# Performance work log

Hardware: AMD Instinct MI355X
Metric: run time of the kernel (lower is better)

Reference implementation:

```python
import jax, jax.numpy as jnp
import numpy as np

HIDDEN = 4096
N_HEADS = 32
HEAD_DIM = HIDDEN // N_HEADS  # 128
ROPE_BASE = 10000.0
NEG_INF = -1e9  # stands in for torch.finfo(dtype).min in the additive mask


def rotate_half(x):
    x1 = x[..., : x.shape[-1] // 2]
    x2 = x[..., x.shape[-1] // 2 :]
    return jnp.concatenate((-x2, x1), axis=-1)


def rope_tables(seq_len, dtype=jnp.float32):
    # RotaryEmbedding: inv_freq = 1/base^(arange(0,dim,2)/dim); emb = cat(freqs, freqs)
    inv_freq = 1.0 / (ROPE_BASE ** (jnp.arange(0, HEAD_DIM, 2, dtype=jnp.float32) / HEAD_DIM))
    t = jnp.arange(seq_len, dtype=jnp.float32)
    freqs = jnp.einsum('s,d->sd', t, inv_freq)          # [S, HEAD_DIM/2]
    emb = jnp.concatenate((freqs, freqs), axis=-1)      # [S, HEAD_DIM]
    return jnp.cos(emb).astype(dtype), jnp.sin(emb).astype(dtype)


def setup_inputs() -> dict:
    key = jax.random.key(0)
    k0, k1, k2 = jax.random.split(key, 3)
    B, S = 1, 2048
    hidden_states = jax.random.normal(k0, (B, S, HIDDEN), dtype=jnp.float32)
    W_pack = jax.random.normal(k1, (3 * HIDDEN, HIDDEN), dtype=jnp.float32) * 0.02
    W_o = jax.random.normal(k2, (HIDDEN, HIDDEN), dtype=jnp.float32) * 0.02
    position_ids = jnp.broadcast_to(jnp.arange(S, dtype=jnp.int32)[None, :], (B, S))
    # additive causal mask [B, 1, S, S]
    causal = jnp.tril(jnp.ones((S, S), dtype=bool))
    attention_mask = jnp.where(causal, 0.0, NEG_INF).astype(jnp.float32)[None, None, :, :]
    attention_mask = jnp.broadcast_to(attention_mask, (B, 1, S, S))
    return {
        'hidden_states': hidden_states,
        'attention_mask': attention_mask,
        'position_ids': position_ids,
        'W_pack': W_pack,
        'W_o': W_o,
    }


def reference(hidden_states, attention_mask, position_ids, W_pack, W_o):
    B, S, H = hidden_states.shape
    norm_factor = 1.0 / np.sqrt(HEAD_DIM)

    # fused QKV projection: Linear(H, 3H, bias=False)
    proj = jnp.einsum('bsh,ph->bsp', hidden_states, W_pack)        # [B, S, 3H]
    q, k, v = jnp.split(proj, 3, axis=-1)

    def to_heads(x):
        return x.reshape(B, S, N_HEADS, HEAD_DIM).transpose(0, 2, 1, 3)  # [B, nH, S, D]

    q, k, v = to_heads(q), to_heads(k), to_heads(v)

    # RoPE (gather per position_ids, matching apply_rotary_pos_emb with unsqueeze_dim=1)
    cos_t, sin_t = rope_tables(S, hidden_states.dtype)
    cos = cos_t[position_ids][:, None, :, :]  # [B, 1, S, D]
    sin = sin_t[position_ids][:, None, :, :]
    q = q * cos + rotate_half(q) * sin
    k = k * cos + rotate_half(k) * sin

    # manual QK^T / softmax / AV (prefill: KV-cache update is a plain copy of cur)
    scores = jnp.einsum('bhqd,bhkd->bhqk', q, k) * norm_factor + attention_mask
    probs = jax.nn.softmax(scores, axis=-1)
    attn = jnp.einsum('bhqk,bhkd->bhqd', probs, v)                 # [B, nH, S, D]

    attn = attn.transpose(0, 2, 1, 3).reshape(B, S, H)
    return jnp.einsum('bsh,oh->bso', attn, W_o)
```

## Files before the change

### kernel.cpp

```cpp
#include <hip/hip_runtime.h>
#include <math.h>

typedef __bf16 bf16x8 __attribute__((ext_vector_type(8)));
typedef __bf16 bf16x4 __attribute__((ext_vector_type(4)));
typedef float f32x4 __attribute__((ext_vector_type(4)));

#define S_LEN 2048
#define NHEADS 32
#define DHEAD 128
#define HID 4096

__device__ __forceinline__ void gld16(const void* g, void* l) {
  __builtin_amdgcn_global_load_lds(
      (const __attribute__((address_space(1))) unsigned int*)g,
      (__attribute__((address_space(3))) unsigned int*)l, 16, 0, 0);
}

__global__ __launch_bounds__(256) void cvt_k(const float4* __restrict__ in,
                                             __bf16* __restrict__ out, int n4) {
  int i = blockIdx.x * 256 + threadIdx.x;
  if (i >= n4) return;
  float4 f = in[i];
  bf16x4 o;
  o[0] = (__bf16)f.x; o[1] = (__bf16)f.y; o[2] = (__bf16)f.z; o[3] = (__bf16)f.w;
  *(bf16x4*)(out + (size_t)i * 4) = o;
}

template <int ND, int KD, int EPI>
__global__ __launch_bounds__(256) void gemm_bt(const __bf16* __restrict__ A,
                                               const __bf16* __restrict__ B,
                                               float* __restrict__ C,
                                               __bf16* __restrict__ Qh,
                                               __bf16* __restrict__ Kh,
                                               __bf16* __restrict__ Vh) {
  const int bn = blockIdx.x, bm = blockIdx.y;
  const int t = threadIdx.x;
  const int w = t >> 6, l = t & 63, quad = l >> 4, l15 = l & 15;
  const int wr = w >> 1, wc = w & 1;

  __shared__ __align__(16) __bf16 As[128 * 32];
  __shared__ __align__(16) __bf16 Bs[128 * 32];

  const f32x4 zero4 = {0.f, 0.f, 0.f, 0.f};
  f32x4 acc[4][4];
#pragma unroll
  for (int i = 0; i < 4; ++i)
#pragma unroll
    for (int j = 0; j < 4; ++j) acc[i][j] = zero4;

  const __bf16* Ab = A + (size_t)bm * 128 * KD;
  const __bf16* Bb = B + (size_t)bn * 128 * KD;

  for (int k0 = 0; k0 < KD; k0 += 32) {
    __syncthreads();
#pragma unroll
    for (int j = 0; j < 2; ++j) {
      const int c = j * 256 + t;
      const int row = c >> 2, kcs = c & 3;
      const int kc = (kcs - (row >> 1)) & 3;
      const int cb = j * 256 + w * 64;
      gld16(Ab + (size_t)row * KD + k0 + kc * 8, As + (size_t)cb * 8);
      gld16(Bb + (size_t)row * KD + k0 + kc * 8, Bs + (size_t)cb * 8);
    }
    __syncthreads();
    bf16x8 af[4], bf_[4];
    const int cq = (quad + (l15 >> 1)) & 3;
#pragma unroll
    for (int mi = 0; mi < 4; ++mi)
      af[mi] = *(const bf16x8*)(As + (wr * 64 + mi * 16 + l15) * 32 + cq * 8);
#pragma unroll
    for (int ni = 0; ni < 4; ++ni)
      bf_[ni] = *(const bf16x8*)(Bs + (wc * 64 + ni * 16 + l15) * 32 + cq * 8);
#pragma unroll
    for (int mi = 0; mi < 4; ++mi)
#pragma unroll
      for (int ni = 0; ni < 4; ++ni)
        acc[mi][ni] = __builtin_amdgcn_mfma_f32_16x16x32_bf16(af[mi], bf_[ni], acc[mi][ni], 0, 0, 0);
  }

#pragma unroll
  for (int mi = 0; mi < 4; ++mi)
#pragma unroll
    for (int ni = 0; ni < 4; ++ni)
#pragma unroll
      for (int r = 0; r < 4; ++r) {
        const int row = bm * 128 + wr * 64 + mi * 16 + quad * 4 + r;
        const int col = bn * 128 + wc * 64 + ni * 16 + l15;
        const float v = acc[mi][ni][r];
        if constexpr (EPI == 0) {
          C[(size_t)row * ND + col] = v;
        } else {
          const int part = col >> 12;
          const int cl = col & 4095;
          const int hh = cl >> 7, d = cl & 127;
          __bf16* dst = (part == 0) ? Qh : (part == 1) ? Kh : Vh;
          dst[(size_t)(hh * S_LEN + row) * DHEAD + d] = (__bf16)v;
        }
      }
}

__global__ __launch_bounds__(256) void rope_k(__bf16* __restrict__ Q, __bf16* __restrict__ K) {
  const int idx = blockIdx.x * 256 + threadIdx.x;
  const int i = idx & 63;
  const int s = (idx >> 6) & (S_LEN - 1);
  const int h = idx >> 17;
  const float inv_freq = __expf(-9.210340371976184f * (float)i * (1.0f / 64.0f));
  float sn, cs;
  sincosf((float)s * inv_freq, &sn, &cs);
  const float nf = 0.08838834764831845f;
  const size_t base = (size_t)(h * S_LEN + s) * DHEAD;
  const float q0 = (float)Q[base + i], q1 = (float)Q[base + i + 64];
  Q[base + i]      = (__bf16)((q0 * cs - q1 * sn) * nf);
  Q[base + i + 64] = (__bf16)((q1 * cs + q0 * sn) * nf);
  const float k0 = (float)K[base + i], k1 = (float)K[base + i + 64];
  K[base + i]      = (__bf16)(k0 * cs - k1 * sn);
  K[base + i + 64] = (__bf16)(k1 * cs + k0 * sn);
}

__global__ __launch_bounds__(256) void vtrans_k(const __bf16* __restrict__ Vh,
                                                __bf16* __restrict__ Vt) {
  __shared__ __align__(16) __bf16 tile[64][72];
  const int s0 = blockIdx.x * 64, d0 = blockIdx.y * 64, h = blockIdx.z;
  const int t = threadIdx.x;
#pragma unroll
  for (int j = 0; j < 2; ++j) {
    const int idx = j * 256 + t;
    const int r = idx >> 3, c8 = idx & 7;
    const bf16x8 v = *(const bf16x8*)(Vh + (size_t)(h * S_LEN + s0 + r) * DHEAD + d0 + c8 * 8);
    *(bf16x8*)(&tile[r][c8 * 8]) = v;
  }
  __syncthreads();
#pragma unroll
  for (int j = 0; j < 2; ++j) {
    const int idx = j * 256 + t;
    const int rd = idx >> 3, c8 = idx & 7;
    bf16x8 v;
#pragma unroll
    for (int i = 0; i < 8; ++i) v[i] = tile[c8 * 8 + i][rd];
    *(bf16x8*)(Vt + (size_t)(h * DHEAD + d0 + rd) * S_LEN + s0 + c8 * 8) = v;
  }
}

__global__ __launch_bounds__(256) void flash_k(const __bf16* __restrict__ Qh,
                                               const __bf16* __restrict__ Kh,
                                               const __bf16* __restrict__ Vt,
                                               __bf16* __restrict__ ctx) {
  const int qt = (int)gridDim.x - 1 - (int)blockIdx.x;
  const int h = blockIdx.y;
  const int t = threadIdx.x;
  const int w = t >> 6, l = t & 63, quad = l >> 4, l15 = l & 15;

  __shared__ __align__(16) __bf16 Ks[64 * 128];
  __shared__ __align__(16) __bf16 Vts[128 * 64];
  __shared__ __align__(16) __bf16 Ps[4][32 * 76];

  const int q0 = qt * 128;
  const int qbase = q0 + w * 32;

  bf16x8 qf[2][4];
#pragma unroll
  for (int mi = 0; mi < 2; ++mi)
#pragma unroll
    for (int ks = 0; ks < 4; ++ks)
      qf[mi][ks] = *(const bf16x8*)(Qh + (size_t)(h * S_LEN + qbase + mi * 16 + l15) * DHEAD +
                                    ks * 32 + quad * 8);

  const f32x4 zero4 = {0.f, 0.f, 0.f, 0.f};
  f32x4 o[2][8];
  float rs[2][4];
#pragma unroll
  for (int mi = 0; mi < 2; ++mi) {
#pragma unroll
    for (int ni = 0; ni < 8; ++ni) o[mi][ni] = zero4;
#pragma unroll
    for (int r = 0; r < 4; ++r) rs[mi][r] = 0.f;
  }

  const int nkt = 2 * (qt + 1);
  for (int kt = 0; kt < nkt; ++kt) {
    const int k0 = kt * 64;
    __syncthreads();
#pragma unroll
    for (int j = 0; j < 4; ++j) {
      const int c = j * 256 + t;
      const int row = c >> 4, dcs = c & 15;
      const int dc = (dcs - row) & 15;
      gld16(Kh + (size_t)(h * S_LEN + k0 + row) * DHEAD + dc * 8,
            Ks + (size_t)(j * 256 + w * 64) * 8);
    }
#pragma unroll
    for (int j = 0; j < 4; ++j) {
      const int c = j * 256 + t;
      const int d = c >> 3, kcs = c & 7;
      const int kc = (kcs - d) & 7;
      gld16(Vt + (size_t)(h * DHEAD + d) * S_LEN + k0 + kc * 8,
            Vts + (size_t)(j * 256 + w * 64) * 8);
    }
    __syncthreads();

    if (k0 <= qbase + 31) {
      f32x4 sacc[2][4];
#pragma unroll
      for (int mi = 0; mi < 2; ++mi)
#pragma unroll
        for (int ni = 0; ni < 4; ++ni) sacc[mi][ni] = zero4;
#pragma unroll
      for (int ks = 0; ks < 4; ++ks) {
        bf16x8 bk[4];
#pragma unroll
        for (int ni = 0; ni < 4; ++ni)
          bk[ni] = *(const bf16x8*)(Ks + (ni * 16 + l15) * 128 +
                                    ((ks * 4 + quad + l15) & 15) * 8);
#pragma unroll
        for (int mi = 0; mi < 2; ++mi)
#pragma unroll
          for (int ni = 0; ni < 4; ++ni)
            sacc[mi][ni] = __builtin_amdgcn_mfma_f32_16x16x32_bf16(qf[mi][ks], bk[ni],
                                                                   sacc[mi][ni], 0, 0, 0);
      }

      const bool need_mask = (k0 + 63 > qbase);
      if (need_mask) {
#pragma unroll
        for (int mi = 0; mi < 2; ++mi)
#pragma unroll
          for (int ni = 0; ni < 4; ++ni)
#pragma unroll
            for (int r = 0; r < 4; ++r) {
              float p = __expf(sacc[mi][ni][r]);
              if (k0 + ni * 16 + l15 > qbase + mi * 16 + quad * 4 + r) p = 0.f;
              rs[mi][r] += p;
              Ps[w][(mi * 16 + quad * 4 + r) * 76 + ni * 16 + l15] = (__bf16)p;
            }
      } else {
#pragma unroll
        for (int mi = 0; mi < 2; ++mi)
#pragma unroll
          for (int ni = 0; ni < 4; ++ni)
#pragma unroll
            for (int r = 0; r < 4; ++r) {
              const float p = __expf(sacc[mi][ni][r]);
              rs[mi][r] += p;
              Ps[w][(mi * 16 + quad * 4 + r) * 76 + ni * 16 + l15] = (__bf16)p;
            }
      }

#pragma unroll
      for (int ks = 0; ks < 2; ++ks) {
        bf16x8 ap[2];
#pragma unroll
        for (int mi = 0; mi < 2; ++mi)
          ap[mi] = *(const bf16x8*)(&Ps[w][(mi * 16 + l15) * 76 + ks * 32 + quad * 8]);
#pragma unroll
        for (int ni = 0; ni < 8; ++ni) {
          const bf16x8 bv = *(const bf16x8*)(Vts + (ni * 16 + l15) * 64 +
                                             ((ks * 4 + quad + l15) & 7) * 8);
#pragma unroll
          for (int mi = 0; mi < 2; ++mi)
            o[mi][ni] = __builtin_amdgcn_mfma_f32_16x16x32_bf16(ap[mi], bv, o[mi][ni], 0, 0, 0);
        }
      }
    }
  }

#pragma unroll
  for (int mi = 0; mi < 2; ++mi)
#pragma unroll
    for (int r = 0; r < 4; ++r) {
      float s = rs[mi][r];
#pragma unroll
      for (int off = 1; off < 16; off <<= 1) s += __shfl_xor(s, off);
      const float inv = 1.f / s;
      const size_t row = (size_t)qbase + mi * 16 + quad * 4 + r;
#pragma unroll
      for (int ni = 0; ni < 8; ++ni)
        ctx[row * HID + h * DHEAD + ni * 16 + l15] = (__bf16)(o[mi][ni][r] * inv);
    }
}

extern "C" void kernel_launch(void* const* d_in, const int* in_sizes, int n_in,
                              void* d_out, int out_size, void* d_ws, size_t ws_size,
                              hipStream_t stream) {
  const float* hs = (const float*)d_in[0];
  const float* Wp = (const float*)d_in[3];
  const float* Wo = (const float*)d_in[4];
  float* out = (float*)d_out;

  char* p = (char*)d_ws;
  auto carve = [&](size_t elems) {
    __bf16* r = (__bf16*)p;
    p += ((elems * sizeof(__bf16) + 255) / 256) * 256;
    return r;
  };
  __bf16* Xb  = carve((size_t)S_LEN * HID);
  __bf16* Wpb = carve((size_t)3 * HID * HID);
  __bf16* Wob = carve((size_t)HID * HID);
  __bf16* Qh  = carve((size_t)S_LEN * HID);
  __bf16* Kh  = carve((size_t)S_LEN * HID);
  __bf16* Vh  = carve((size_t)S_LEN * HID);
  __bf16* Vt  = carve((size_t)S_LEN * HID);
  __bf16* ctx = carve((size_t)S_LEN * HID);

  cvt_k<<<(S_LEN * HID / 4) / 256, 256, 0, stream>>>((const float4*)hs, Xb, S_LEN * HID / 4);
  cvt_k<<<(3 * HID * HID / 4) / 256, 256, 0, stream>>>((const float4*)Wp, Wpb, 3 * HID * HID / 4);
  cvt_k<<<(HID * HID / 4) / 256, 256, 0, stream>>>((const float4*)Wo, Wob, HID * HID / 4);

  gemm_bt<3 * HID, HID, 1><<<dim3(96, 16), 256, 0, stream>>>(Xb, Wpb, nullptr, Qh, Kh, Vh);
  rope_k<<<(NHEADS * S_LEN * 64) / 256, 256, 0, stream>>>(Qh, Kh);
  vtrans_k<<<dim3(S_LEN / 64, DHEAD / 64, NHEADS), 256, 0, stream>>>(Vh, Vt);
  flash_k<<<dim3(S_LEN / 128, NHEADS), 256, 0, stream>>>(Qh, Kh, Vt, ctx);
  gemm_bt<HID, HID, 0><<<dim3(32, 16), 256, 0, stream>>>(ctx, Wob, out, nullptr, nullptr, nullptr);
}
```

Baseline: 851.3 us.

## Add 256x256-tile 8-wave QKV GEMM with XCD swizzle and quadrant pipelining

Replaces the 128x128-tile QKV projection GEMM with a new kernel that uses 256x256 output tiles, 512 threads, and double-buffered LDS staged via direct global-to-LDS loads. It staggers A and B prefetch across four MFMA quadrants with barriers and priority hints, and swizzles block indices across XCDs for L2 locality. The larger tiles are meant to raise arithmetic intensity and cut global traffic, in exchange for heavy LDS use (128KB) and register pressure that limit occupancy.

```diff
diff --git a/kernel.cpp b/kernel.cpp
--- a/kernel.cpp
+++ b/kernel.cpp
@@ -96,6 +96,162 @@
           __bf16* dst = (part == 0) ? Qh : (part == 1) ? Kh : Vh;
           dst[(size_t)(hh * S_LEN + row) * DHEAD + d] = (__bf16)v;
         }
+      }
+}
+
+template <int ND, int KD>
+__global__ __launch_bounds__(512, 2) void gemm256_qkv(const __bf16* __restrict__ A,
+                                                      const __bf16* __restrict__ B,
+                                                      __bf16* __restrict__ Qh,
+                                                      __bf16* __restrict__ Kh,
+                                                      __bf16* __restrict__ Vh) {
+  constexpr int NB = ND / 256;
+  constexpr int MB = S_LEN / 256;
+  constexpr int KT = KD / 64;
+  constexpr int NWG = NB * MB;
+  static_assert(NWG % 8 == 0, "XCD swizzle needs nwg % 8 == 0");
+
+  const int lin = (int)blockIdx.y * NB + (int)blockIdx.x;
+  const int swz = (lin & 7) * (NWG / 8) + (lin >> 3);
+  const int bm = swz / NB, bn = swz % NB;
+
+  const int t = threadIdx.x;
+  const int w = t >> 6, l = t & 63, quad = l >> 4, l15 = l & 15;
+  const int wr = w >> 2, wc = w & 3;
+
+  __shared__ __align__(16) __bf16 As[2][256 * 64];
+  __shared__ __align__(16) __bf16 Bs[2][256 * 64];
+
+  const __bf16* Ab = A + (size_t)bm * 256 * KD;
+  const __bf16* Bb = B + (size_t)bn * 256 * KD;
+
+  const f32x4 zero4 = {0.f, 0.f, 0.f, 0.f};
+  f32x4 acc[8][4];
+#pragma unroll
+  for (int i = 0; i < 8; ++i)
+#pragma unroll
+    for (int j = 0; j < 4; ++j) acc[i][j] = zero4;
+
+  auto stageA = [&](int buf, int h, int k0) {
+#pragma unroll
+    for (int j = 0; j < 2; ++j) {
+      const int cc = j * 512 + t;
+      const int row = cc >> 3;
+      const int c = ((cc & 7) - (row >> 1)) & 7;
+      gld16(Ab + (size_t)(h * 128 + row) * KD + k0 + c * 8,
+            &As[buf][h * 8192 + (j * 512 + w * 64) * 8]);
+    }
+  };
+  auto stageB = [&](int buf, int h, int k0) {
+#pragma unroll
+    for (int j = 0; j < 2; ++j) {
+      const int cc = j * 512 + t;
+      const int row = cc >> 3;
+      const int c = ((cc & 7) - (row >> 1)) & 7;
+      gld16(Bb + (size_t)(h * 128 + row) * KD + k0 + c * 8,
+            &Bs[buf][h * 8192 + (j * 512 + w * 64) * 8]);
+    }
+  };
+
+  stageA(0, 0, 0); stageA(0, 1, 0);
+  stageB(0, 0, 0); stageB(0, 1, 0);
+  stageB(1, 0, 64); stageB(1, 1, 64);
+  asm volatile("s_waitcnt vmcnt(4)" ::: "memory");
+  __builtin_amdgcn_s_barrier();
+
+  bf16x8 afr[4][2];
+  bf16x8 bfr[4][2];
+
+  auto loadA = [&](const __bf16* LA, int qm) {
+#pragma unroll
+    for (int mi4 = 0; mi4 < 4; ++mi4)
+#pragma unroll
+      for (int ks = 0; ks < 2; ++ks) {
+        const int R = wr * 128 + qm * 64 + mi4 * 16 + l15;
+        const int slot = (ks * 4 + quad + (l15 >> 1)) & 7;
+        afr[mi4][ks] = *(const bf16x8*)(LA + (size_t)R * 64 + slot * 8);
+      }
+  };
+  auto loadB = [&](const __bf16* LB, int qn) {
+#pragma unroll
+    for (int n2 = 0; n2 < 2; ++n2)
+#pragma unroll
+      for (int ks = 0; ks < 2; ++ks) {
+        const int ni = qn * 2 + n2;
+        const int R = wc * 64 + ni * 16 + l15;
+        const int slot = (ks * 4 + quad + (l15 >> 1)) & 7;
+        bfr[ni][ks] = *(const bf16x8*)(LB + (size_t)R * 64 + slot * 8);
+      }
+  };
+  auto mmaq = [&](int qm, int qn) {
+    __builtin_amdgcn_s_setprio(1);
+#pragma unroll
+    for (int ks = 0; ks < 2; ++ks)
+#pragma unroll
+      for (int mi4 = 0; mi4 < 4; ++mi4)
+#pragma unroll
+        for (int n2 = 0; n2 < 2; ++n2)
+          acc[qm * 4 + mi4][qn * 2 + n2] = __builtin_amdgcn_mfma_f32_16x16x32_bf16(
+              afr[mi4][ks], bfr[qn * 2 + n2][ks], acc[qm * 4 + mi4][qn * 2 + n2], 0, 0, 0);
+    __builtin_amdgcn_s_setprio(0);
+  };
+
+#pragma unroll 1
+  for (int t0 = 0; t0 < KT; t0 += 2) {
+#pragma unroll
+    for (int hf = 0; hf < 2; ++hf) {
+      const int tt = t0 + hf;
+      const __bf16* LA = &As[hf][0];
+      const __bf16* LB = &Bs[hf][0];
+      const bool sA = (tt + 1) < KT;
+      const bool sB = (tt + 2) < KT;
+      const int kA = (tt + 1) * 64, kB = (tt + 2) * 64;
+
+      loadA(LA, 0);
+      loadB(LB, 0);
+      if (sA) stageA(hf ^ 1, 0, kA);
+      __builtin_amdgcn_s_barrier();
+      asm volatile("s_waitcnt lgkmcnt(0)" ::: "memory");
+      mmaq(0, 0);
+      __builtin_amdgcn_s_barrier();
+      loadB(LB, 1);
+      if (sA) stageA(hf ^ 1, 1, kA);
+      __builtin_amdgcn_s_barrier();
+      asm volatile("s_waitcnt lgkmcnt(0)" ::: "memory");
+      mmaq(0, 1);
+      __builtin_amdgcn_s_barrier();
+      loadA(LA, 1);
+      if (sB) stageB(hf, 0, kB);
+      __builtin_amdgcn_s_barrier();
+      asm volatile("s_waitcnt lgkmcnt(0)" ::: "memory");
+      mmaq(1, 0);
+      __builtin_amdgcn_s_barrier();
+      if (sB) {
+        stageB(hf, 1, kB);
+        asm volatile("s_waitcnt vmcnt(4)" ::: "memory");
+      } else {
+        asm volatile("s_waitcnt vmcnt(0)" ::: "memory");
+      }
+      __builtin_amdgcn_s_barrier();
+      mmaq(1, 1);
+      __builtin_amdgcn_s_barrier();
+    }
+  }
+
+#pragma unroll
+  for (int mi = 0; mi < 8; ++mi)
+#pragma unroll
+    for (int ni = 0; ni < 4; ++ni)
+#pragma unroll
+      for (int r = 0; r < 4; ++r) {
+        const int row = bm * 256 + wr * 128 + mi * 16 + quad * 4 + r;
+        const int col = bn * 256 + wc * 64 + ni * 16 + l15;
+        const float v = acc[mi][ni][r];
+        const int part = col >> 12;
+        const int cl = col & 4095;
+        const int hh = cl >> 7, d = cl & 127;
+        __bf16* dst = (part == 0) ? Qh : (part == 1) ? Kh : Vh;
+        dst[(size_t)(hh * S_LEN + row) * DHEAD + d] = (__bf16)v;
       }
 }
 
@@ -305,7 +461,7 @@
   cvt_k<<<(3 * HID * HID / 4) / 256, 256, 0, stream>>>((const float4*)Wp, Wpb, 3 * HID * HID / 4);
   cvt_k<<<(HID * HID / 4) / 256, 256, 0, stream>>>((const float4*)Wo, Wob, HID * HID / 4);
 
-  gemm_bt<3 * HID, HID, 1><<<dim3(96, 16), 256, 0, stream>>>(Xb, Wpb, nullptr, Qh, Kh, Vh);
+  gemm256_qkv<3 * HID, HID><<<dim3(48, 8), 512, 0, stream>>>(Xb, Wpb, Qh, Kh, Vh);
   rope_k<<<(NHEADS * S_LEN * 64) / 256, 256, 0, stream>>>(Qh, Kh);
   vtrans_k<<<dim3(S_LEN / 64, DHEAD / 64, NHEADS), 256, 0, stream>>>(Vh, Vt);
   flash_k<<<dim3(S_LEN / 128, NHEADS), 256, 0, stream>>>(Qh, Kh, Vt, ctx);
```

Result: slower. 884.1 us (+3.8%).
